# Optimization experiments

Measured on AMD Instinct MI355X. Metric: run time of the kernel, lower is better.

Reference implementation:

```python
import jax, jax.numpy as jnp
import numpy as np

B, N, D = 16, 1024, 768
SCALE = D ** (-0.5)


def setup_inputs() -> dict:
    key = jax.random.key(0)
    ks = jax.random.split(key, 6)
    return {
        "x": jax.random.normal(ks[0], (B, N, D), dtype=jnp.float32),
        "y": jax.random.normal(ks[1], (B, N, D), dtype=jnp.float32),
        "coords": jax.random.normal(ks[2], (N, N, 6), dtype=jnp.float32),
        "W_qk": jax.random.normal(ks[3], (D, D), dtype=jnp.float32) * (D ** -0.5),
        "pos_emb": jax.random.normal(ks[4], (N, 6, 1), dtype=jnp.float32) * 0.02,
        "gating": jnp.float32(1.0),
        "temp": jnp.float32(0.1),
    }


def reference(x, y, coords, W_qk, pos_emb, gating, temp):
    # k = Linear(y), no bias; torch Linear: y @ W.T
    k = jnp.einsum('bnd,ed->bne', y, W_qk)
    # content score [B, N, N]
    patch_score = jax.nn.softmax(jnp.einsum('bnd,bmd->bnm', x, k) * SCALE, axis=-1)
    # positional score: coords [N, N, 6] @ pos_emb [N, 6, 1] -> [N, N]
    pos_score = jax.nn.softmax(jnp.einsum('pnk,pkl->pnl', coords, pos_emb)[..., 0], axis=-1)
    g = jax.nn.sigmoid(gating)
    attn = (1.0 - g) * patch_score + g * pos_score[None, :, :]  # broadcast over B
    out = jnp.einsum('bnm,bmd->bnd', attn, y)
    entropy = jnp.sum(-attn * jnp.log(attn + 1e-8), axis=-1, keepdims=True)  # [B, N, 1]
    hmap = 2.0 * (1.0 - jax.nn.sigmoid(temp * entropy))
    return out, hmap
```

## Files before the change

kernel.cpp:

```cpp
#include <hip/hip_runtime.h>
#include <hip/hip_bf16.h>
#include <cstdint>

typedef __bf16 bf16_t;
typedef __bf16 bf16x8 __attribute__((ext_vector_type(8)));
typedef __bf16 bf16x4 __attribute__((ext_vector_type(4)));
typedef float f32x4 __attribute__((ext_vector_type(4)));

static constexpr int B = 16, N = 1024, D = 768;
static constexpr float SCALE = 0.03608439182435161f;

#define ASYNC_COPY16(gptr, lptr)                                                          \
  __builtin_amdgcn_global_load_lds((const __attribute__((address_space(1))) void*)(gptr), \
                                   (__attribute__((address_space(3))) void*)(lptr), 16, 0, 0)

__device__ __forceinline__ float wave_red_max(float v) {
#pragma unroll
  for (int o = 32; o > 0; o >>= 1) v = fmaxf(v, __shfl_down(v, o, 64));
  return v;
}
__device__ __forceinline__ float wave_red_sum(float v) {
#pragma unroll
  for (int o = 32; o > 0; o >>= 1) v += __shfl_down(v, o, 64);
  return v;
}
__device__ __forceinline__ float block_max(float v, float* sm) {
  v = wave_red_max(v);
  int lane = threadIdx.x & 63, w = threadIdx.x >> 6;
  if (lane == 0) sm[w] = v;
  __syncthreads();
  return fmaxf(fmaxf(sm[0], sm[1]), fmaxf(sm[2], sm[3]));
}
__device__ __forceinline__ float block_sum(float v, float* sm) {
  v = wave_red_sum(v);
  int lane = threadIdx.x & 63, w = threadIdx.x >> 6;
  if (lane == 0) sm[w] = v;
  __syncthreads();
  return sm[0] + sm[1] + sm[2] + sm[3];
}

__global__ __launch_bounds__(256) void cast_f32_bf16_4(const float4* __restrict__ in,
                                                       bf16x4* __restrict__ out, int n4) {
  int i = blockIdx.x * 256 + threadIdx.x;
  if (i < n4) {
    float4 v = in[i];
    bf16x4 o;
    o.x = (bf16_t)v.x; o.y = (bf16_t)v.y; o.z = (bf16_t)v.z; o.w = (bf16_t)v.w;
    out[i] = o;
  }
}

__global__ __launch_bounds__(256) void transpose_bf16(const bf16_t* __restrict__ in,
                                                      bf16_t* __restrict__ out) {
  __shared__ bf16_t t[32][33];
  int b = blockIdx.z;
  int d0 = blockIdx.x * 32;
  int n0 = blockIdx.y * 32;
  int tx = threadIdx.x & 31;
  int ty = threadIdx.x >> 5;
  const bf16_t* src = in + (size_t)b * N * D;
  bf16_t* dst = out + (size_t)b * N * D;
#pragma unroll
  for (int r = 0; r < 4; r++) {
    int n = n0 + ty + r * 8;
    t[ty + r * 8][tx] = src[(size_t)n * D + d0 + tx];
  }
  __syncthreads();
#pragma unroll
  for (int r = 0; r < 4; r++) {
    int d = d0 + ty + r * 8;
    dst[(size_t)d * N + n0 + tx] = t[tx][ty + r * 8];
  }
}

__global__ __launch_bounds__(256) void pos_softmax_k(const float* __restrict__ coords,
                                                     const float* __restrict__ pemb,
                                                     float* __restrict__ pos) {
  __shared__ float sm1[4], sm2[4];
  int p = blockIdx.x;
  int tid = threadIdx.x;
  float e[6];
#pragma unroll
  for (int k = 0; k < 6; k++) e[k] = pemb[p * 6 + k];
  float v[4];
#pragma unroll
  for (int i = 0; i < 4; i++) {
    int n = tid + i * 256;
    const float* c = coords + ((size_t)p * N + n) * 6;
    float s = 0.f;
#pragma unroll
    for (int k = 0; k < 6; k++) s += c[k] * e[k];
    v[i] = s;
  }
  float m = block_max(fmaxf(fmaxf(v[0], v[1]), fmaxf(v[2], v[3])), sm1);
  float ex[4], ls = 0.f;
#pragma unroll
  for (int i = 0; i < 4; i++) { ex[i] = __expf(v[i] - m); ls += ex[i]; }
  float sum = block_sum(ls, sm2);
  float inv = 1.f / sum;
#pragma unroll
  for (int i = 0; i < 4; i++) pos[(size_t)p * N + tid + i * 256] = ex[i] * inv;
}

__global__ __launch_bounds__(256) void attn_entropy_k(float* __restrict__ S,
                                                      const float* __restrict__ pos,
                                                      const float* __restrict__ gating,
                                                      const float* __restrict__ temp,
                                                      float* __restrict__ hmap) {
  __shared__ float sm1[4], sm2[4], sm3[4];
  size_t row = blockIdx.x;
  int q = (int)(row & (size_t)(N - 1));
  int tid = threadIdx.x;
  float* Srow = S + row * N;
  float g = 1.f / (1.f + __expf(-gating[0]));
  float s[4];
#pragma unroll
  for (int i = 0; i < 4; i++) s[i] = Srow[tid + i * 256];
  float m = block_max(fmaxf(fmaxf(s[0], s[1]), fmaxf(s[2], s[3])), sm1);
  float e[4], ls = 0.f;
#pragma unroll
  for (int i = 0; i < 4; i++) { e[i] = __expf(s[i] - m); ls += e[i]; }
  float sum = block_sum(ls, sm2);
  float inv = 1.f / sum;
  const float* prow = pos + (size_t)q * N;
  float a[4], ent = 0.f;
#pragma unroll
  for (int i = 0; i < 4; i++) {
    float patch = e[i] * inv;
    float ps = prow[tid + i * 256];
    a[i] = (1.f - g) * patch + g * ps;
    ent += -a[i] * __logf(a[i] + 1e-8f);
  }
  float E = block_sum(ent, sm3);
  __syncthreads();
  bf16_t* arow = (bf16_t*)Srow;
#pragma unroll
  for (int i = 0; i < 4; i++) arow[tid + i * 256] = (bf16_t)a[i];
  if (tid == 0) hmap[row] = 2.f / (1.f + __expf(temp[0] * E));
}

template <typename OutT>
__global__ __launch_bounds__(512) void gemm_nt_256(const bf16_t* __restrict__ A, int lda, long long sA,
                                                   const bf16_t* __restrict__ Bm, int ldb, long long sB,
                                                   OutT* __restrict__ C, int ldc, long long sC,
                                                   int K, float scale, int swz) {
  __shared__ __align__(16) char lds_raw[49152];
  bf16_t* As = (bf16_t*)lds_raw;
  bf16_t* Bs = (bf16_t*)(lds_raw + 32768);

  const int tid = threadIdx.x;
  const int lane = tid & 63, wave = tid >> 6;
  const int wr = wave >> 1, wc = wave & 1;
  const int quad = lane >> 4, lr = lane & 15;

  int bx = blockIdx.x, by = blockIdx.y, bz = blockIdx.z;
  if (swz) {
    int Gx = gridDim.x, Gy = gridDim.y, Gz = gridDim.z;
    int i = bx + Gx * (by + Gy * bz);
    int xcd = i & 7, slot = i >> 3;
    int T = Gx * Gy;
    int bpx = Gz >> 3;
    bz = xcd * bpx + slot / T;
    int t = slot % T;
    bx = t % Gx;
    by = t / Gx;
  }
  const int tileN = bx * 128, tileM = by * 256;
  A += (long long)bz * sA + (long long)tileM * lda;
  Bm += (long long)bz * sB + (long long)tileN * ldb;
  C += (long long)bz * sC;

  const bf16_t* ag = A + (long long)(wave * 32 + (lane >> 3)) * lda + (lane & 7) * 8;
  const bf16_t* bg = Bm + (long long)(wave * 16 + (lane >> 3)) * ldb + (lane & 7) * 8;

  f32x4 acc[4][4];
#pragma unroll
  for (int i = 0; i < 4; i++)
#pragma unroll
    for (int j = 0; j < 4; j++) acc[i][j] = (f32x4){0.f, 0.f, 0.f, 0.f};

  for (int kt = 0; kt < K; kt += 64) {
#pragma unroll
    for (int i = 0; i < 4; i++)
      ASYNC_COPY16(ag + (long long)i * 8 * lda + kt, &As[(wave * 32 + i * 8) * 64]);
#pragma unroll
    for (int i = 0; i < 2; i++)
      ASYNC_COPY16(bg + (long long)i * 8 * ldb + kt, &Bs[(wave * 16 + i * 8) * 64]);
    __syncthreads();
#pragma unroll
    for (int kk = 0; kk < 2; kk++) {
      bf16x8 af[4], bfr[4];
#pragma unroll
      for (int i = 0; i < 4; i++) {
        af[i] = *(const bf16x8*)&As[(wr * 64 + i * 16 + lr) * 64 + kk * 32 + quad * 8];
        bfr[i] = *(const bf16x8*)&Bs[(wc * 64 + i * 16 + lr) * 64 + kk * 32 + quad * 8];
      }
#pragma unroll
      for (int mi = 0; mi < 4; mi++)
#pragma unroll
        for (int nj = 0; nj < 4; nj++)
          acc[mi][nj] = __builtin_amdgcn_mfma_f32_16x16x32_bf16(af[mi], bfr[nj], acc[mi][nj], 0, 0, 0);
    }
    __syncthreads();
  }

  float* epi = (float*)lds_raw + wave * (16 * 68);
#pragma unroll
  for (int mi = 0; mi < 4; mi++) {
#pragma unroll
    for (int nj = 0; nj < 4; nj++)
#pragma unroll
      for (int r = 0; r < 4; r++)
        epi[(quad * 4 + r) * 68 + nj * 16 + lr] = acc[mi][nj][r] * scale;
    if constexpr (sizeof(OutT) == 4) {
#pragma unroll
      for (int seg = 0; seg < 4; seg++) {
        int lrow = seg * 4 + (lane >> 4);
        f32x4 v = *(const f32x4*)&epi[lrow * 68 + (lane & 15) * 4];
        long long grow = tileM + wr * 64 + mi * 16 + lrow;
        int gcol = tileN + wc * 64 + (lane & 15) * 4;
        *(f32x4*)&C[grow * ldc + gcol] = v;
      }
    } else {
#pragma unroll
      for (int seg = 0; seg < 2; seg++) {
        int lrow = seg * 8 + (lane >> 3);
        const float* p = &epi[lrow * 68 + (lane & 7) * 8];
        f32x4 v0 = *(const f32x4*)&p[0];
        f32x4 v1 = *(const f32x4*)&p[4];
        bf16x8 o;
#pragma unroll
        for (int j = 0; j < 4; j++) { o[j] = (bf16_t)v0[j]; o[j + 4] = (bf16_t)v1[j]; }
        long long grow = tileM + wr * 64 + mi * 16 + lrow;
        int gcol = tileN + wc * 64 + (lane & 7) * 8;
        *(bf16x8*)&C[grow * ldc + gcol] = o;
      }
    }
  }
}

extern "C" void kernel_launch(void* const* d_in, const int* in_sizes, int n_in,
                              void* d_out, int out_size, void* d_ws, size_t ws_size,
                              hipStream_t stream) {
  const float* x = (const float*)d_in[0];
  const float* y = (const float*)d_in[1];
  const float* coords = (const float*)d_in[2];
  const float* W = (const float*)d_in[3];
  const float* pemb = (const float*)d_in[4];
  const float* gating = (const float*)d_in[5];
  const float* temp = (const float*)d_in[6];
  float* out = (float*)d_out;
  float* hmap = out + (size_t)B * N * D;

  char* ws = (char*)d_ws;
  bf16_t* xb = (bf16_t*)(ws + 0);
  bf16_t* yb = (bf16_t*)(ws + 25165824);
  bf16_t* yT = (bf16_t*)(ws + 50331648);
  bf16_t* Wb = (bf16_t*)(ws + 75497472);
  bf16_t* kb = (bf16_t*)(ws + 76677120);
  float* pos = (float*)(ws + 101842944);
  float* S   = (float*)(ws + 106037248);

  const int BND = B * N * D;

  cast_f32_bf16_4<<<BND / 4 / 256, 256, 0, stream>>>((const float4*)x, (bf16x4*)xb, BND / 4);
  cast_f32_bf16_4<<<BND / 4 / 256, 256, 0, stream>>>((const float4*)y, (bf16x4*)yb, BND / 4);
  cast_f32_bf16_4<<<(D * D / 4 + 255) / 256, 256, 0, stream>>>((const float4*)W, (bf16x4*)Wb, D * D / 4);
  transpose_bf16<<<dim3(D / 32, N / 32, B), 256, 0, stream>>>(yb, yT);
  pos_softmax_k<<<N, 256, 0, stream>>>(coords, pemb, pos);

  gemm_nt_256<bf16_t><<<dim3(D / 128, (B * N) / 256, 1), 512, 0, stream>>>(
      yb, D, 0LL, Wb, D, 0LL, kb, D, 0LL, D, 1.0f, 0);

  gemm_nt_256<float><<<dim3(N / 128, N / 256, B), 512, 0, stream>>>(
      xb, D, (long long)N * D, kb, D, (long long)N * D, S, N, (long long)N * N, D, SCALE, 1);

  attn_entropy_k<<<B * N, 256, 0, stream>>>(S, pos, gating, temp, hmap);

  gemm_nt_256<float><<<dim3(D / 128, N / 256, B), 512, 0, stream>>>(
      (const bf16_t*)S, 2 * N, (long long)N * 2 * N, yT, N, (long long)N * D, out, D, (long long)N * D, N, 1.0f, 1);
}
```

Measured before the change: 325.4 us.

## Double-buffer GEMM LDS tiles and fuse y cast with transpose

The GEMM kernel now uses two LDS buffers (96 KB total). It issues async global-to-LDS loads for the next K tile while computing on the current one, so one barrier per iteration overlaps load latency with MFMA work. Separately, the y cast to bf16 and the transpose are fused into one kernel that reads fp32 y once and writes both the row-major and transposed bf16 copies, removing a full pass over y. The larger LDS footprint may reduce occupancy, and the fused kernel's row-major bf16 stores are narrow 2-byte writes.

```diff
diff --git a/kernel.cpp b/kernel.cpp
--- a/kernel.cpp
+++ b/kernel.cpp
@@ -50,26 +50,31 @@
   }
 }
 
-__global__ __launch_bounds__(256) void transpose_bf16(const bf16_t* __restrict__ in,
-                                                      bf16_t* __restrict__ out) {
+__global__ __launch_bounds__(256) void cast_transpose_y(const float* __restrict__ y,
+                                                        bf16_t* __restrict__ yb,
+                                                        bf16_t* __restrict__ yT) {
   __shared__ bf16_t t[32][33];
   int b = blockIdx.z;
   int d0 = blockIdx.x * 32;
   int n0 = blockIdx.y * 32;
   int tx = threadIdx.x & 31;
   int ty = threadIdx.x >> 5;
-  const bf16_t* src = in + (size_t)b * N * D;
-  bf16_t* dst = out + (size_t)b * N * D;
+  const float* src = y + (size_t)b * N * D;
+  bf16_t* dstN = yb + (size_t)b * N * D;
+  bf16_t* dstT = yT + (size_t)b * N * D;
 #pragma unroll
   for (int r = 0; r < 4; r++) {
     int n = n0 + ty + r * 8;
-    t[ty + r * 8][tx] = src[(size_t)n * D + d0 + tx];
+    float v = src[(size_t)n * D + d0 + tx];
+    bf16_t h = (bf16_t)v;
+    t[ty + r * 8][tx] = h;
+    dstN[(size_t)n * D + d0 + tx] = h;
   }
   __syncthreads();
 #pragma unroll
   for (int r = 0; r < 4; r++) {
     int d = d0 + ty + r * 8;
-    dst[(size_t)d * N + n0 + tx] = t[tx][ty + r * 8];
+    dstT[(size_t)d * N + n0 + tx] = t[tx][ty + r * 8];
   }
 }
 
@@ -144,9 +149,7 @@
                                                    const bf16_t* __restrict__ Bm, int ldb, long long sB,
                                                    OutT* __restrict__ C, int ldc, long long sC,
                                                    int K, float scale, int swz) {
-  __shared__ __align__(16) char lds_raw[49152];
-  bf16_t* As = (bf16_t*)lds_raw;
-  bf16_t* Bs = (bf16_t*)(lds_raw + 32768);
+  __shared__ __align__(16) char lds_raw[98304];
 
   const int tid = threadIdx.x;
   const int lane = tid & 63, wave = tid >> 6;
@@ -179,14 +182,30 @@
 #pragma unroll
     for (int j = 0; j < 4; j++) acc[i][j] = (f32x4){0.f, 0.f, 0.f, 0.f};
 
-  for (int kt = 0; kt < K; kt += 64) {
-#pragma unroll
-    for (int i = 0; i < 4; i++)
-      ASYNC_COPY16(ag + (long long)i * 8 * lda + kt, &As[(wave * 32 + i * 8) * 64]);
-#pragma unroll
-    for (int i = 0; i < 2; i++)
-      ASYNC_COPY16(bg + (long long)i * 8 * ldb + kt, &Bs[(wave * 16 + i * 8) * 64]);
-    __syncthreads();
+  const int nk = K >> 6;
+
+#pragma unroll
+  for (int i = 0; i < 4; i++)
+    ASYNC_COPY16(ag + (long long)i * 8 * lda, lds_raw + (wave * 32 + i * 8) * 128);
+#pragma unroll
+  for (int i = 0; i < 2; i++)
+    ASYNC_COPY16(bg + (long long)i * 8 * ldb, lds_raw + 32768 + (wave * 16 + i * 8) * 128);
+  __syncthreads();
+
+  int cur = 0;
+  for (int t = 0; t < nk; ++t) {
+    if (t + 1 < nk) {
+      char* nb = lds_raw + ((cur ^ 1) * 49152);
+      const int kt = (t + 1) << 6;
+#pragma unroll
+      for (int i = 0; i < 4; i++)
+        ASYNC_COPY16(ag + (long long)i * 8 * lda + kt, nb + (wave * 32 + i * 8) * 128);
+#pragma unroll
+      for (int i = 0; i < 2; i++)
+        ASYNC_COPY16(bg + (long long)i * 8 * ldb + kt, nb + 32768 + (wave * 16 + i * 8) * 128);
+    }
+    const bf16_t* As = (const bf16_t*)(lds_raw + cur * 49152);
+    const bf16_t* Bs = (const bf16_t*)(lds_raw + cur * 49152 + 32768);
 #pragma unroll
     for (int kk = 0; kk < 2; kk++) {
       bf16x8 af[4], bfr[4];
@@ -202,6 +221,7 @@
           acc[mi][nj] = __builtin_amdgcn_mfma_f32_16x16x32_bf16(af[mi], bfr[nj], acc[mi][nj], 0, 0, 0);
     }
     __syncthreads();
+    cur ^= 1;
   }
 
   float* epi = (float*)lds_raw + wave * (16 * 68);
@@ -264,9 +284,8 @@
   const int BND = B * N * D;
 
   cast_f32_bf16_4<<<BND / 4 / 256, 256, 0, stream>>>((const float4*)x, (bf16x4*)xb, BND / 4);
-  cast_f32_bf16_4<<<BND / 4 / 256, 256, 0, stream>>>((const float4*)y, (bf16x4*)yb, BND / 4);
   cast_f32_bf16_4<<<(D * D / 4 + 255) / 256, 256, 0, stream>>>((const float4*)W, (bf16x4*)Wb, D * D / 4);
-  transpose_bf16<<<dim3(D / 32, N / 32, B), 256, 0, stream>>>(yb, yT);
+  cast_transpose_y<<<dim3(D / 32, N / 32, B), 256, 0, stream>>>(y, yb, yT);
   pos_softmax_k<<<N, 256, 0, stream>>>(coords, pemb, pos);
 
   gemm_nt_256<bf16_t><<<dim3(D / 128, (B * N) / 256, 1), 512, 0, stream>>>(
```

Result: slower. 341.1 us (+4.9%).
